# Kernel optimization log

Measured on AMD Instinct MI355X. Metric: run time of the kernel, lower is better.

## Reference

```python
import jax, jax.numpy as jnp
import numpy as np

B, S, DIN, DOUT = 4, 2048, 4096, 4096

def setup_inputs() -> dict:
    key = jax.random.key(0)
    k1, k2, k3 = jax.random.split(key, 3)
    x = jax.random.normal(k1, (B, S, DIN), dtype=jnp.float32)
    # symmetric int8 quantized weights, [out_features, in_features]
    int_weight = jax.random.randint(k2, (DOUT, DIN), -128, 128, dtype=jnp.int32).astype(jnp.int8)
    w_scale = jnp.float32(0.01)  # per-tensor scale, zero-point = 0
    fp_bias = jax.random.normal(k3, (DOUT,), dtype=jnp.float32) * 0.01
    return {"x": x, "int_weight": int_weight, "w_scale": w_scale, "fp_bias": fp_bias}

def reference(x, int_weight, w_scale, fp_bias):
    # Dequantize weight: fp32 = int8 * scale (elementwise), then F.linear: x @ w.T + b
    w = int_weight.astype(jnp.float32) * w_scale  # [DOUT, DIN]
    out = jnp.einsum('bsi,oi->bso', x, w) + fp_bias
    return out
```

## Files before the change

kernel.cpp:

```cpp
#include <hip/hip_runtime.h>
#include <hip/hip_bf16.h>

typedef __attribute__((ext_vector_type(8))) short bf16x8;
typedef __attribute__((ext_vector_type(4))) float f32x4;
typedef __attribute__((ext_vector_type(4))) int i32x4;
typedef __attribute__((ext_vector_type(2))) unsigned int u32x2;
typedef __attribute__((ext_vector_type(4))) unsigned int u32x4;

__device__ __forceinline__ unsigned int f2bf(float f) {
    union { float f; unsigned int u; } v; v.f = f;
    unsigned int u = v.u;
    u += 0x7FFFu + ((u >> 16) & 1u);
    return u >> 16;
}

__device__ __forceinline__ void gl_lds16(const void* gptr, void* lptr) {
    __builtin_amdgcn_global_load_lds(
        (const __attribute__((address_space(1))) unsigned int*)gptr,
        (__attribute__((address_space(3))) unsigned int*)lptr, 16, 0, 0);
}

__global__ __launch_bounds__(256) void convert_x_kernel(
    const float* __restrict__ x, unsigned short* __restrict__ xb, long long n8)
{
    long long i = (long long)blockIdx.x * blockDim.x + threadIdx.x;
    const long long stride = (long long)gridDim.x * blockDim.x;
    for (; i < n8; i += stride) {
        const f32x4* p = (const f32x4*)(x + i * 8);
        f32x4 v0 = p[0], v1 = p[1];
        u32x4 q;
        q[0] = f2bf(v0[0]) | (f2bf(v0[1]) << 16);
        q[1] = f2bf(v0[2]) | (f2bf(v0[3]) << 16);
        q[2] = f2bf(v1[0]) | (f2bf(v1[1]) << 16);
        q[3] = f2bf(v1[2]) | (f2bf(v1[3]) << 16);
        *(u32x4*)(xb + i * 8) = q;
    }
}

__global__ __launch_bounds__(256) void convert_w_kernel(
    const int* __restrict__ w, unsigned short* __restrict__ wb, long long n8)
{
    long long i = (long long)blockIdx.x * blockDim.x + threadIdx.x;
    const long long stride = (long long)gridDim.x * blockDim.x;
    for (; i < n8; i += stride) {
        const i32x4* p = (const i32x4*)(w + i * 8);
        i32x4 v0 = p[0], v1 = p[1];
        u32x4 q;
        q[0] = f2bf((float)v0[0]) | (f2bf((float)v0[1]) << 16);
        q[1] = f2bf((float)v0[2]) | (f2bf((float)v0[3]) << 16);
        q[2] = f2bf((float)v1[0]) | (f2bf((float)v1[1]) << 16);
        q[3] = f2bf((float)v1[2]) | (f2bf((float)v1[3]) << 16);
        *(u32x4*)(wb + i * 8) = q;
    }
}

__global__ __launch_bounds__(512, 2) void gemm256_kernel(
    const unsigned short* __restrict__ A, const unsigned short* __restrict__ Bw,
    const float* __restrict__ wscale, const float* __restrict__ bias,
    float* __restrict__ out, int M, int N, int K)
{
    __shared__ unsigned char lds[131072];

    const int tid  = threadIdx.x;
    const int lane = tid & 63;
    const int wid  = tid >> 6;
    const int wr   = wid >> 1;
    const int wc   = wid & 1;

    const int ntn = N >> 8;
    const int nwg = gridDim.x;
    int bid = blockIdx.x;
    if ((nwg & 7) == 0) {
        const int cpx = nwg >> 3;
        bid = (bid & 7) * cpx + (bid >> 3);
    }
    const int bm = bid / ntn;
    const int bn = bid % ntn;
    const int NT = K >> 6;

    const char* Abase = (const char*)(A  + (size_t)bm * 256 * K);
    const char* Bbase = (const char*)(Bw + (size_t)bn * 256 * K);
    const size_t rowb = (size_t)K * 2;

    const int s_colb = (((lane & 7) ^ (lane >> 3)) << 4);
    const int s_rsub = wid * 8 + (lane >> 3);
    const int s_ldso = wid * 1024 + lane * 16;

    auto stageHalf = [&](const char* gRowBase, char* lhalf) {
#pragma unroll
        for (int q = 0; q < 2; ++q)
            gl_lds16(gRowBase + (size_t)(q * 64 + s_rsub) * rowb + s_colb,
                     lhalf + q * 8192 + s_ldso);
    };
    auto Ag = [&](int kt, int h) { return Abase + (size_t)kt * 128 + (size_t)(h * 128) * rowb; };
    auto Bg = [&](int kt, int h) { return Bbase + (size_t)kt * 128 + (size_t)(h * 128) * rowb; };

    const int arow = (wr * 64  + (lane & 15)) * 128;
    const int brow = (wc * 128 + (lane & 15)) * 128;
    const int csw0 = (((lane >> 4) * 16))      ^ ((lane & 7) << 4);
    const int csw1 = (((lane >> 4) * 16) + 64) ^ ((lane & 7) << 4);

    f32x4 acc[4][8];
#pragma unroll
    for (int mi = 0; mi < 4; ++mi)
#pragma unroll
        for (int ni = 0; ni < 8; ++ni)
            acc[mi][ni] = (f32x4){0.f, 0.f, 0.f, 0.f};

    stageHalf(Ag(0, 0), (char*)lds + 0);
    stageHalf(Ag(0, 1), (char*)lds + 16384);
    stageHalf(Bg(0, 0), (char*)lds + 32768);
    stageHalf(Bg(0, 1), (char*)lds + 49152);
    if (NT > 1) {
        stageHalf(Ag(1, 0), (char*)lds + 65536);
        stageHalf(Ag(1, 1), (char*)lds + 65536 + 16384);
        asm volatile("s_waitcnt vmcnt(4)" ::: "memory");
    } else {
        asm volatile("s_waitcnt vmcnt(0)" ::: "memory");
    }
    __builtin_amdgcn_sched_barrier(0);
    asm volatile("s_barrier" ::: "memory");

#pragma unroll 2
    for (int kt = 0; kt < NT; ++kt) {
        const int c = kt & 1;
        const char* Al = (const char*)lds + (c << 16);
        const char* Bl = Al + 32768;
        char* nbuf = (char*)lds + ((c ^ 1) << 16);
        char* cbuf = (char*)lds + (c << 16);
        bf16x8 a0[4], a1[4], b[4], b2[4];

#pragma unroll
        for (int fm = 0; fm < 4; ++fm) a0[fm] = *(const bf16x8*)(Al + arow + fm * 16 * 128 + csw0);
#pragma unroll
        for (int fn = 0; fn < 4; ++fn) b[fn]  = *(const bf16x8*)(Bl + brow + fn * 16 * 128 + csw0);
        if (kt + 1 < NT) stageHalf(Bg(kt + 1, 0), nbuf + 32768);
        asm volatile("s_barrier" ::: "memory");
        __builtin_amdgcn_s_setprio(1);
#pragma unroll
        for (int fm = 0; fm < 4; ++fm)
#pragma unroll
            for (int fn = 0; fn < 4; ++fn)
                acc[fm][fn] = __builtin_amdgcn_mfma_f32_16x16x32_bf16(a0[fm], b[fn], acc[fm][fn], 0, 0, 0);
        __builtin_amdgcn_s_setprio(0);
        asm volatile("s_barrier" ::: "memory");

#pragma unroll
        for (int fm = 0; fm < 4; ++fm) a1[fm] = *(const bf16x8*)(Al + arow + fm * 16 * 128 + csw1);
#pragma unroll
        for (int fn = 0; fn < 4; ++fn) b2[fn] = *(const bf16x8*)(Bl + brow + (fn + 4) * 16 * 128 + csw0);
        if (kt + 1 < NT) stageHalf(Bg(kt + 1, 1), nbuf + 49152);
        asm volatile("s_barrier" ::: "memory");
        __builtin_amdgcn_s_setprio(1);
#pragma unroll
        for (int fm = 0; fm < 4; ++fm)
#pragma unroll
            for (int fn = 0; fn < 4; ++fn)
                acc[fm][fn + 4] = __builtin_amdgcn_mfma_f32_16x16x32_bf16(a0[fm], b2[fn], acc[fm][fn + 4], 0, 0, 0);
        __builtin_amdgcn_s_setprio(0);
        asm volatile("s_waitcnt lgkmcnt(0)" ::: "memory");
        asm volatile("s_barrier" ::: "memory");

#pragma unroll
        for (int fn = 0; fn < 4; ++fn) b[fn]  = *(const bf16x8*)(Bl + brow + fn * 16 * 128 + csw1);
#pragma unroll
        for (int fn = 0; fn < 4; ++fn) b2[fn] = *(const bf16x8*)(Bl + brow + (fn + 4) * 16 * 128 + csw1);
        if (kt + 2 < NT) stageHalf(Ag(kt + 2, 0), cbuf);
        asm volatile("s_barrier" ::: "memory");
        __builtin_amdgcn_s_setprio(1);
#pragma unroll
        for (int fm = 0; fm < 4; ++fm)
#pragma unroll
            for (int fn = 0; fn < 4; ++fn)
                acc[fm][fn] = __builtin_amdgcn_mfma_f32_16x16x32_bf16(a1[fm], b[fn], acc[fm][fn], 0, 0, 0);
        __builtin_amdgcn_s_setprio(0);
        asm volatile("s_barrier" ::: "memory");

        if (kt + 2 < NT) stageHalf(Ag(kt + 2, 1), cbuf + 16384);
        asm volatile("s_barrier" ::: "memory");
        __builtin_amdgcn_s_setprio(1);
#pragma unroll
        for (int fm = 0; fm < 4; ++fm)
#pragma unroll
            for (int fn = 0; fn < 4; ++fn)
                acc[fm][fn + 4] = __builtin_amdgcn_mfma_f32_16x16x32_bf16(a1[fm], b2[fn], acc[fm][fn + 4], 0, 0, 0);
        __builtin_amdgcn_s_setprio(0);
        if (kt + 2 < NT) { asm volatile("s_waitcnt vmcnt(4)" ::: "memory"); }
        else             { asm volatile("s_waitcnt vmcnt(0)" ::: "memory"); }
        __builtin_amdgcn_sched_barrier(0);
        asm volatile("s_barrier" ::: "memory");
    }

    const float scale = *wscale;
    const int orow0 = bm * 256 + wr * 64  + ((lane >> 4) << 2);
    const int ocol0 = bn * 256 + wc * 128 + (lane & 15);
#pragma unroll
    for (int fn = 0; fn < 8; ++fn) {
        const int col = ocol0 + 16 * fn;
        const float bb = bias[col];
#pragma unroll
        for (int fm = 0; fm < 4; ++fm) {
            const int row0 = orow0 + 16 * fm;
#pragma unroll
            for (int i = 0; i < 4; ++i)
                out[(size_t)(row0 + i) * N + col] = acc[fm][fn][i] * scale + bb;
        }
    }
}

__device__ __forceinline__ int swz(int row, int byte_in_row) {
    return row * 128 + (byte_in_row ^ ((row & 7) << 4));
}

__global__ __launch_bounds__(256) void qlinear_fused_kernel(
    const float* __restrict__ X, const int* __restrict__ W,
    const float* __restrict__ wscale, const float* __restrict__ bias,
    float* __restrict__ out, int M, int N, int K)
{
    __shared__ unsigned char smem[32768];

    const int t    = threadIdx.x;
    const int lane = t & 63;
    const int wid  = t >> 6;
    const int wr   = wid >> 1;
    const int wc   = wid & 1;

    const int ntn = N >> 7;
    const int bm  = blockIdx.x / ntn;
    const int bn  = blockIdx.x % ntn;
    const int NT  = K >> 6;

    const float* Ab = X + (size_t)bm * 128 * K;
    const int*   Bb = W + (size_t)bn * 128 * K;

    const int srow = t >> 4, sc4 = t & 15;

    f32x4 av[8];
    i32x4 bv[8];

    auto loadAB = [&](int kt) {
        const float* Ap = Ab + kt * 64 + sc4 * 4;
#pragma unroll
        for (int l = 0; l < 8; ++l)
            av[l] = *(const f32x4*)(Ap + (size_t)(srow + 16 * l) * K);
        const int* Bp = Bb + kt * 64 + sc4 * 4;
#pragma unroll
        for (int l = 0; l < 8; ++l)
            bv[l] = *(const i32x4*)(Bp + (size_t)(srow + 16 * l) * K);
    };

    auto writeAB = [&]() {
#pragma unroll
        for (int l = 0; l < 8; ++l) {
            const int row = srow + 16 * l;
            u32x2 pk;
            pk[0] = f2bf(av[l][0]) | (f2bf(av[l][1]) << 16);
            pk[1] = f2bf(av[l][2]) | (f2bf(av[l][3]) << 16);
            *(u32x2*)(smem + swz(row, sc4 * 8)) = pk;
        }
#pragma unroll
        for (int l = 0; l < 8; ++l) {
            const int row = srow + 16 * l;
            u32x2 pk;
            pk[0] = f2bf((float)bv[l][0]) | (f2bf((float)bv[l][1]) << 16);
            pk[1] = f2bf((float)bv[l][2]) | (f2bf((float)bv[l][3]) << 16);
            *(u32x2*)(smem + 16384 + swz(row, sc4 * 8)) = pk;
        }
    };

    f32x4 acc[4][4];
#pragma unroll
    for (int mi = 0; mi < 4; ++mi)
#pragma unroll
        for (int ni = 0; ni < 4; ++ni)
            acc[mi][ni] = (f32x4){0.f, 0.f, 0.f, 0.f};

    const int kbyte = (lane >> 4) * 16;
    const int afr   = wr * 64 + (lane & 15);
    const int bfr   = wc * 64 + (lane & 15);

    loadAB(0);

    for (int kt = 0; kt < NT; ++kt) {
        writeAB();
        __syncthreads();
        if (kt + 1 < NT) loadAB(kt + 1);
#pragma unroll
        for (int kk = 0; kk < 2; ++kk) {
            bf16x8 a[4], b[4];
#pragma unroll
            for (int mi = 0; mi < 4; ++mi)
                a[mi] = *(const bf16x8*)(smem + swz(afr + 16 * mi, kk * 64 + kbyte));
#pragma unroll
            for (int ni = 0; ni < 4; ++ni)
                b[ni] = *(const bf16x8*)(smem + 16384 + swz(bfr + 16 * ni, kk * 64 + kbyte));
#pragma unroll
            for (int mi = 0; mi < 4; ++mi)
#pragma unroll
                for (int ni = 0; ni < 4; ++ni)
                    acc[mi][ni] = __builtin_amdgcn_mfma_f32_16x16x32_bf16(
                        a[mi], b[ni], acc[mi][ni], 0, 0, 0);
        }
        __syncthreads();
    }

    const float scale = *wscale;
    const int orow0 = bm * 128 + wr * 64 + ((lane >> 4) << 2);
    const int ocol0 = bn * 128 + wc * 64 + (lane & 15);
#pragma unroll
    for (int ni = 0; ni < 4; ++ni) {
        const int col = ocol0 + 16 * ni;
        const float bb = bias[col];
#pragma unroll
        for (int mi = 0; mi < 4; ++mi) {
            const int row0 = orow0 + 16 * mi;
#pragma unroll
            for (int i = 0; i < 4; ++i)
                out[(size_t)(row0 + i) * N + col] = acc[mi][ni][i] * scale + bb;
        }
    }
}

extern "C" void kernel_launch(void* const* d_in, const int* in_sizes, int n_in,
                              void* d_out, int out_size, void* d_ws, size_t ws_size,
                              hipStream_t stream) {
    const float* x      = (const float*)d_in[0];
    const int*   w      = (const int*)d_in[1];
    const float* wscale = (const float*)d_in[2];
    const float* bias   = (const float*)d_in[3];
    float*       out    = (float*)d_out;

    const int DOUT = in_sizes[3];
    const int DIN  = in_sizes[1] / DOUT;
    const int M    = in_sizes[0] / DIN;

    const size_t xb_bytes = (size_t)M * DIN * 2;
    const size_t wb_bytes = (size_t)DOUT * DIN * 2;

    if (ws_size >= xb_bytes + wb_bytes && (M % 256) == 0 && (DOUT % 256) == 0) {
        unsigned short* xb = (unsigned short*)d_ws;
        unsigned short* wb = (unsigned short*)((char*)d_ws + xb_bytes);

        const long long nx8 = (long long)M * DIN / 8;
        const long long nw8 = (long long)DOUT * DIN / 8;
        convert_x_kernel<<<2048, 256, 0, stream>>>(x, xb, nx8);
        convert_w_kernel<<<2048, 256, 0, stream>>>(w, wb, nw8);

        dim3 grid((M / 256) * (DOUT / 256));
        gemm256_kernel<<<grid, 512, 0, stream>>>(xb, wb, wscale, bias, out, M, DOUT, DIN);
    } else {
        dim3 grid((M / 128) * (DOUT / 128));
        qlinear_fused_kernel<<<grid, 256, 0, stream>>>(x, w, wscale, bias, out, M, DOUT, DIN);
    }
}
```

Measured before the change: 292.7 us.

## Software-pipeline LDS fragment loads across MFMA phases and drop barriers

Restructures the main K loop so each phase's LDS fragment reads are issued before the previous phase's MFMAs, double-buffering registers (a0/a1, bA/bB) and prefetching the next tile's first fragments at the end of the iteration. Removes several per-phase s_barriers, aiming to hide LDS latency behind matrix math and cut synchronisation stalls. It raises register pressure and depends on the rearranged vmcnt waits and barriers still ordering LDS writes and reads correctly.

```diff
diff --git a/kernel.cpp b/kernel.cpp
--- a/kernel.cpp
+++ b/kernel.cpp
@@ -107,6 +107,8 @@
         for (int ni = 0; ni < 8; ++ni)
             acc[mi][ni] = (f32x4){0.f, 0.f, 0.f, 0.f};
 
+    bf16x8 a0[4], a1[4], bA[4], bB[4];
+
     stageHalf(Ag(0, 0), (char*)lds + 0);
     stageHalf(Ag(0, 1), (char*)lds + 16384);
     stageHalf(Bg(0, 0), (char*)lds + 32768);
@@ -120,74 +122,80 @@
     }
     __builtin_amdgcn_sched_barrier(0);
     asm volatile("s_barrier" ::: "memory");
+    {
+        const char* Al = (const char*)lds;
+        const char* Bl = Al + 32768;
+#pragma unroll
+        for (int fm = 0; fm < 4; ++fm) a0[fm] = *(const bf16x8*)(Al + arow + fm * 2048 + csw0);
+#pragma unroll
+        for (int fn = 0; fn < 4; ++fn) bA[fn] = *(const bf16x8*)(Bl + brow + fn * 2048 + csw0);
+    }
 
 #pragma unroll 2
     for (int kt = 0; kt < NT; ++kt) {
         const int c = kt & 1;
         const char* Al = (const char*)lds + (c << 16);
         const char* Bl = Al + 32768;
-        char* nbuf = (char*)lds + ((c ^ 1) << 16);
-        char* cbuf = (char*)lds + (c << 16);
-        bf16x8 a0[4], a1[4], b[4], b2[4];
-
-#pragma unroll
-        for (int fm = 0; fm < 4; ++fm) a0[fm] = *(const bf16x8*)(Al + arow + fm * 16 * 128 + csw0);
-#pragma unroll
-        for (int fn = 0; fn < 4; ++fn) b[fn]  = *(const bf16x8*)(Bl + brow + fn * 16 * 128 + csw0);
-        if (kt + 1 < NT) stageHalf(Bg(kt + 1, 0), nbuf + 32768);
-        asm volatile("s_barrier" ::: "memory");
+        char* nb = (char*)lds + ((c ^ 1) << 16);
+        char* cb = (char*)lds + (c << 16);
+
+        if (kt + 1 < NT) stageHalf(Bg(kt + 1, 0), nb + 32768);
+#pragma unroll
+        for (int fm = 0; fm < 4; ++fm) a1[fm] = *(const bf16x8*)(Al + arow + fm * 2048 + csw1);
+#pragma unroll
+        for (int fn = 0; fn < 4; ++fn) bB[fn] = *(const bf16x8*)(Bl + brow + (fn + 4) * 2048 + csw0);
         __builtin_amdgcn_s_setprio(1);
 #pragma unroll
         for (int fm = 0; fm < 4; ++fm)
 #pragma unroll
             for (int fn = 0; fn < 4; ++fn)
-                acc[fm][fn] = __builtin_amdgcn_mfma_f32_16x16x32_bf16(a0[fm], b[fn], acc[fm][fn], 0, 0, 0);
+                acc[fm][fn] = __builtin_amdgcn_mfma_f32_16x16x32_bf16(a0[fm], bA[fn], acc[fm][fn], 0, 0, 0);
         __builtin_amdgcn_s_setprio(0);
-        asm volatile("s_barrier" ::: "memory");
-
-#pragma unroll
-        for (int fm = 0; fm < 4; ++fm) a1[fm] = *(const bf16x8*)(Al + arow + fm * 16 * 128 + csw1);
-#pragma unroll
-        for (int fn = 0; fn < 4; ++fn) b2[fn] = *(const bf16x8*)(Bl + brow + (fn + 4) * 16 * 128 + csw0);
-        if (kt + 1 < NT) stageHalf(Bg(kt + 1, 1), nbuf + 49152);
-        asm volatile("s_barrier" ::: "memory");
+
+        if (kt + 1 < NT) stageHalf(Bg(kt + 1, 1), nb + 49152);
+#pragma unroll
+        for (int fn = 0; fn < 4; ++fn) bA[fn] = *(const bf16x8*)(Bl + brow + fn * 2048 + csw1);
         __builtin_amdgcn_s_setprio(1);
 #pragma unroll
         for (int fm = 0; fm < 4; ++fm)
 #pragma unroll
             for (int fn = 0; fn < 4; ++fn)
-                acc[fm][fn + 4] = __builtin_amdgcn_mfma_f32_16x16x32_bf16(a0[fm], b2[fn], acc[fm][fn + 4], 0, 0, 0);
+                acc[fm][fn + 4] = __builtin_amdgcn_mfma_f32_16x16x32_bf16(a0[fm], bB[fn], acc[fm][fn + 4], 0, 0, 0);
         __builtin_amdgcn_s_setprio(0);
         asm volatile("s_waitcnt lgkmcnt(0)" ::: "memory");
         asm volatile("s_barrier" ::: "memory");
 
-#pragma unroll
-        for (int fn = 0; fn < 4; ++fn) b[fn]  = *(const bf16x8*)(Bl + brow + fn * 16 * 128 + csw1);
-#pragma unroll
-        for (int fn = 0; fn < 4; ++fn) b2[fn] = *(const bf16x8*)(Bl + brow + (fn + 4) * 16 * 128 + csw1);
-        if (kt + 2 < NT) stageHalf(Ag(kt + 2, 0), cbuf);
-        asm volatile("s_barrier" ::: "memory");
+        if (kt + 2 < NT) stageHalf(Ag(kt + 2, 0), cb + 0);
+#pragma unroll
+        for (int fn = 0; fn < 4; ++fn) bB[fn] = *(const bf16x8*)(Bl + brow + (fn + 4) * 2048 + csw1);
         __builtin_amdgcn_s_setprio(1);
 #pragma unroll
         for (int fm = 0; fm < 4; ++fm)
 #pragma unroll
             for (int fn = 0; fn < 4; ++fn)
-                acc[fm][fn] = __builtin_amdgcn_mfma_f32_16x16x32_bf16(a1[fm], b[fn], acc[fm][fn], 0, 0, 0);
+                acc[fm][fn] = __builtin_amdgcn_mfma_f32_16x16x32_bf16(a1[fm], bA[fn], acc[fm][fn], 0, 0, 0);
         __builtin_amdgcn_s_setprio(0);
-        asm volatile("s_barrier" ::: "memory");
-
-        if (kt + 2 < NT) stageHalf(Ag(kt + 2, 1), cbuf + 16384);
-        asm volatile("s_barrier" ::: "memory");
+
+        if (kt + 2 < NT) stageHalf(Ag(kt + 2, 1), cb + 16384);
+        if (kt + 1 < NT) {
+            if (kt + 2 < NT) { asm volatile("s_waitcnt vmcnt(4)" ::: "memory"); }
+            else             { asm volatile("s_waitcnt vmcnt(0)" ::: "memory"); }
+            __builtin_amdgcn_sched_barrier(0);
+            asm volatile("s_barrier" ::: "memory");
+            const char* nAl = (const char*)nb;
+            const char* nBl = (const char*)nb + 32768;
+#pragma unroll
+            for (int fm = 0; fm < 4; ++fm) a0[fm] = *(const bf16x8*)(nAl + arow + fm * 2048 + csw0);
+#pragma unroll
+            for (int fn = 0; fn < 4; ++fn) bA[fn] = *(const bf16x8*)(nBl + brow + fn * 2048 + csw0);
+        }
         __builtin_amdgcn_s_setprio(1);
 #pragma unroll
         for (int fm = 0; fm < 4; ++fm)
 #pragma unroll
             for (int fn = 0; fn < 4; ++fn)
-                acc[fm][fn + 4] = __builtin_amdgcn_mfma_f32_16x16x32_bf16(a1[fm], b2[fn], acc[fm][fn + 4], 0, 0, 0);
+                acc[fm][fn + 4] = __builtin_amdgcn_mfma_f32_16x16x32_bf16(a1[fm], bB[fn], acc[fm][fn + 4], 0, 0, 0);
         __builtin_amdgcn_s_setprio(0);
-        if (kt + 2 < NT) { asm volatile("s_waitcnt vmcnt(4)" ::: "memory"); }
-        else             { asm volatile("s_waitcnt vmcnt(0)" ::: "memory"); }
-        __builtin_amdgcn_sched_barrier(0);
         asm volatile("s_barrier" ::: "memory");
     }
 
```

New measurement: 285.8 us. -2.3%, faster.
